# Kernel tuning notes

Hardware: AMD Instinct MI355X
Metric: run time of the kernel (lower is better)

Reference implementation:

```python
import jax, jax.numpy as jnp
import numpy as np

N, D = 65536, 512

def setup_inputs() -> dict:
    key = jax.random.key(0)
    k1, k2, k3, k4, k5 = jax.random.split(key, 5)
    lim = 1.0 / np.sqrt(D)
    inputs = jax.random.normal(k1, (N, D), dtype=jnp.float32)
    key_w = jax.random.uniform(k2, (1, D), minval=-lim, maxval=lim, dtype=jnp.float32)
    key_b = jax.random.uniform(k3, (1,), minval=-lim, maxval=lim, dtype=jnp.float32)
    value_w = jax.random.uniform(k4, (D, D), minval=-lim, maxval=lim, dtype=jnp.float32)
    value_b = jax.random.uniform(k5, (D,), minval=-lim, maxval=lim, dtype=jnp.float32)
    return {"inputs": inputs, "key_w": key_w, "key_b": key_b,
            "value_w": value_w, "value_b": value_b}

def reference(inputs, key_w, key_b, value_w, value_b):
    # key: [N,1], value: [N,D] (torch Linear: x @ W.T + b)
    k = inputs @ key_w.T + key_b            # [N,1]
    v = inputs @ value_w.T + value_b        # [N,D]
    # Reassociate (v @ inputs.T) @ k == v @ (inputs.T @ k): avoids O(N^2) intermediate
    s = inputs.T @ k                        # [D,1]
    x = v @ s                               # [N,1]
    return jax.nn.softmax(x, axis=0)        # softmax over nodes (dim=0)
```

## Files before the change

kernel.cpp:

```cpp
#include <hip/hip_runtime.h>
#include <float.h>

#define NROWS 65536
#define DDIM  512

#define WS_S8   0
#define WS_T    4096
#define WS_M    4608
#define WS_SUM  4609
#define WS_HDR_BYTES ((4610) * 4)

__device__ __forceinline__ unsigned encf(float f) {
    unsigned u = __float_as_uint(f);
    return (u & 0x80000000u) ? ~u : (u | 0x80000000u);
}
__device__ __forceinline__ float decf(unsigned e) {
    unsigned u = (e & 0x80000000u) ? (e ^ 0x80000000u) : ~e;
    return __uint_as_float(u);
}

__global__ __launch_bounds__(256) void kA(const float* __restrict__ in,
                                          const float* __restrict__ key_w,
                                          const float* __restrict__ key_b,
                                          float* __restrict__ s8) {
    const int lane = threadIdx.x & 63;
    const int wv   = threadIdx.x >> 6;
    const int gw   = blockIdx.x * 4 + wv;
    const int nw   = gridDim.x * 4;
    const float4* in4 = (const float4*)in;
    const float4* kw4 = (const float4*)key_w;
    const float4 kw0 = kw4[lane];
    const float4 kw1 = kw4[64 + lane];
    const float  kb  = key_b[0];
    float4 a0 = make_float4(0.f, 0.f, 0.f, 0.f);
    float4 a1 = make_float4(0.f, 0.f, 0.f, 0.f);

    for (int row = gw; row < NROWS; row += nw) {
        const float4* r = in4 + (size_t)row * (DDIM / 4);
        float4 v0 = r[lane];
        float4 v1 = r[64 + lane];
        float p = v0.x*kw0.x + v0.y*kw0.y + v0.z*kw0.z + v0.w*kw0.w
                + v1.x*kw1.x + v1.y*kw1.y + v1.z*kw1.z + v1.w*kw1.w;
        #pragma unroll
        for (int o = 32; o > 0; o >>= 1) p += __shfl_xor(p, o, 64);
        const float k = p + kb;
        a0.x += k*v0.x; a0.y += k*v0.y; a0.z += k*v0.z; a0.w += k*v0.w;
        a1.x += k*v1.x; a1.y += k*v1.y; a1.z += k*v1.z; a1.w += k*v1.w;
    }

    __shared__ float sb[4][512];
    sb[wv][4*lane+0]     = a0.x; sb[wv][4*lane+1]     = a0.y;
    sb[wv][4*lane+2]     = a0.z; sb[wv][4*lane+3]     = a0.w;
    sb[wv][256+4*lane+0] = a1.x; sb[wv][256+4*lane+1] = a1.y;
    sb[wv][256+4*lane+2] = a1.z; sb[wv][256+4*lane+3] = a1.w;
    __syncthreads();

    float* dst = s8 + (size_t)(blockIdx.x & 7) * 512;
    int d = threadIdx.x;
    atomicAdd(&dst[d], sb[0][d] + sb[1][d] + sb[2][d] + sb[3][d]);
    d += 256;
    atomicAdd(&dst[d], sb[0][d] + sb[1][d] + sb[2][d] + sb[3][d]);
}

__global__ __launch_bounds__(512) void kB(const float* __restrict__ vw,
                                          const float* __restrict__ s8,
                                          float* __restrict__ t) {
    const int j = threadIdx.x;
    float acc = 0.f;
    #pragma unroll
    for (int ii = 0; ii < 8; ++ii) {
        const int i = blockIdx.x * 8 + ii;
        float si = 0.f;
        #pragma unroll
        for (int c = 0; c < 8; ++c) si += s8[c * 512 + i];
        acc += vw[(size_t)i * 512 + j] * si;
    }
    atomicAdd(&t[j], acc);
}

__global__ __launch_bounds__(256) void kC(const float* __restrict__ in,
                                          const float* __restrict__ t,
                                          float* __restrict__ x,
                                          unsigned* __restrict__ Menc) {
    const int lane = threadIdx.x & 63;
    const int wv   = threadIdx.x >> 6;
    const int gw   = blockIdx.x * 4 + wv;
    const int nw   = gridDim.x * 4;
    const float4* in4 = (const float4*)in;
    const float4* t4  = (const float4*)t;
    const float4 t0 = t4[lane];
    const float4 t1 = t4[64 + lane];
    float xmax = -FLT_MAX;

    for (int row = gw; row < NROWS; row += nw) {
        const float4* r = in4 + (size_t)row * (DDIM / 4);
        float4 v0 = r[lane];
        float4 v1 = r[64 + lane];
        float p = v0.x*t0.x + v0.y*t0.y + v0.z*t0.z + v0.w*t0.w
                + v1.x*t1.x + v1.y*t1.y + v1.z*t1.z + v1.w*t1.w;
        #pragma unroll
        for (int o = 32; o > 0; o >>= 1) p += __shfl_xor(p, o, 64);
        if (lane == 0) x[row] = p;
        xmax = fmaxf(xmax, p);
    }

    __shared__ float mb[4];
    if (lane == 0) mb[wv] = xmax;
    __syncthreads();
    if (threadIdx.x == 0) {
        float m = fmaxf(fmaxf(mb[0], mb[1]), fmaxf(mb[2], mb[3]));
        atomicMax(Menc, encf(m));
    }
}

__global__ __launch_bounds__(256) void kD(const float* __restrict__ x,
                                          const unsigned* __restrict__ Menc,
                                          float* __restrict__ sum) {
    const float M = decf(*Menc);
    float acc = 0.f;
    for (int i = blockIdx.x * blockDim.x + threadIdx.x; i < NROWS;
         i += gridDim.x * blockDim.x)
        acc += expf(x[i] - M);
    #pragma unroll
    for (int o = 32; o > 0; o >>= 1) acc += __shfl_xor(acc, o, 64);
    __shared__ float sb[4];
    if ((threadIdx.x & 63) == 0) sb[threadIdx.x >> 6] = acc;
    __syncthreads();
    if (threadIdx.x == 0) atomicAdd(sum, sb[0] + sb[1] + sb[2] + sb[3]);
}

__global__ __launch_bounds__(256) void kE(float* __restrict__ x,
                                          const unsigned* __restrict__ Menc,
                                          const float* __restrict__ sum) {
    const float M = decf(*Menc);
    const float inv = 1.0f / *sum;
    for (int i = blockIdx.x * blockDim.x + threadIdx.x; i < NROWS;
         i += gridDim.x * blockDim.x)
        x[i] = expf(x[i] - M) * inv;
}

extern "C" void kernel_launch(void* const* d_in, const int* in_sizes, int n_in,
                              void* d_out, int out_size, void* d_ws, size_t ws_size,
                              hipStream_t stream) {
    const float* in    = (const float*)d_in[0];
    const float* key_w = (const float*)d_in[1];
    const float* key_b = (const float*)d_in[2];
    const float* vw    = (const float*)d_in[3];

    float* ws  = (float*)d_ws;
    float* s8  = ws + WS_S8;
    float* t   = ws + WS_T;
    unsigned* Menc = (unsigned*)(ws + WS_M);
    float* sum = ws + WS_SUM;
    float* x   = (float*)d_out;

    hipMemsetAsync(d_ws, 0, WS_HDR_BYTES, stream);
    kA<<<1024, 256, 0, stream>>>(in, key_w, key_b, s8);
    kB<<<64, 512, 0, stream>>>(vw, s8, t);
    kC<<<1024, 256, 0, stream>>>(in, t, x, Menc);
    kD<<<64, 256, 0, stream>>>(x, Menc, sum);
    kE<<<256, 256, 0, stream>>>(x, Menc, sum);
}
```

Measured before the change: 234.4 us.

## Fuse all stages into one cooperative kernel with grid-wide syncs

Replaces the memset and five separate kernel launches with a single cooperative launch of 1024 blocks that uses grid.sync between phases. Per-block partial sums are written to workspace and reduced deterministically instead of through atomics, and each block handles a contiguous chunk of rows. Launch gaps and the memset are removed, in exchange for several grid-wide barriers, a 1024x512 partial buffer that must be reduced, and a grid that must be fully co-resident. The later phases also switch expf to __expf.

Result: slower. 767.3 us (+227.4%).

```diff
diff --git a/kernel.cpp b/kernel.cpp
--- a/kernel.cpp
+++ b/kernel.cpp
@@ -1,14 +1,14 @@
 #include <hip/hip_runtime.h>
+#include <hip/hip_cooperative_groups.h>
 #include <float.h>
+
+namespace cg = cooperative_groups;
 
 #define NROWS 65536
 #define DDIM  512
+#define NBLK  1024
+#define ROWS_PER_BLK (NROWS / NBLK)
 
-#define WS_S8   0
-#define WS_T    4096
-#define WS_M    4608
-#define WS_SUM  4609
-#define WS_HDR_BYTES ((4610) * 4)
 
 __device__ __forceinline__ unsigned encf(float f) {
     unsigned u = __float_as_uint(f);
@@ -19,124 +19,141 @@
     return __uint_as_float(u);
 }
 
-__global__ __launch_bounds__(256) void kA(const float* __restrict__ in,
-                                          const float* __restrict__ key_w,
-                                          const float* __restrict__ key_b,
-                                          float* __restrict__ s8) {
-    const int lane = threadIdx.x & 63;
-    const int wv   = threadIdx.x >> 6;
-    const int gw   = blockIdx.x * 4 + wv;
-    const int nw   = gridDim.x * 4;
+__global__ __launch_bounds__(256, 4) void fused(const float* __restrict__ in,
+                                                const float* __restrict__ key_w,
+                                                const float* __restrict__ key_b,
+                                                const float* __restrict__ vw,
+                                                float* __restrict__ ws,
+                                                float* __restrict__ out) {
+    cg::grid_group grid = cg::this_grid();
+    const int tid  = threadIdx.x;
+    const int lane = tid & 63;
+    const int wv   = tid >> 6;
+    const int blk  = blockIdx.x;
+
+    float*    spart = ws;
+    float*    s     = ws + (size_t)NBLK * DDIM;
+    float*    t     = s + DDIM;
+    unsigned* Menc  = (unsigned*)(t + DDIM);
+    float*    sum   = (float*)(Menc + 1);
+
+    __shared__ float sb[4][DDIM];
+    __shared__ float red[4];
+
     const float4* in4 = (const float4*)in;
-    const float4* kw4 = (const float4*)key_w;
-    const float4 kw0 = kw4[lane];
-    const float4 kw1 = kw4[64 + lane];
-    const float  kb  = key_b[0];
-    float4 a0 = make_float4(0.f, 0.f, 0.f, 0.f);
-    float4 a1 = make_float4(0.f, 0.f, 0.f, 0.f);
+    const int base = blk * ROWS_PER_BLK;
 
-    for (int row = gw; row < NROWS; row += nw) {
-        const float4* r = in4 + (size_t)row * (DDIM / 4);
-        float4 v0 = r[lane];
-        float4 v1 = r[64 + lane];
-        float p = v0.x*kw0.x + v0.y*kw0.y + v0.z*kw0.z + v0.w*kw0.w
-                + v1.x*kw1.x + v1.y*kw1.y + v1.z*kw1.z + v1.w*kw1.w;
-        #pragma unroll
-        for (int o = 32; o > 0; o >>= 1) p += __shfl_xor(p, o, 64);
-        const float k = p + kb;
-        a0.x += k*v0.x; a0.y += k*v0.y; a0.z += k*v0.z; a0.w += k*v0.w;
-        a1.x += k*v1.x; a1.y += k*v1.y; a1.z += k*v1.z; a1.w += k*v1.w;
+    {
+        const float4* kw4 = (const float4*)key_w;
+        const float4 kw0 = kw4[lane];
+        const float4 kw1 = kw4[64 + lane];
+        const float  kb  = key_b[0];
+        float4 a0 = make_float4(0.f, 0.f, 0.f, 0.f);
+        float4 a1 = make_float4(0.f, 0.f, 0.f, 0.f);
+        for (int i = 0; i < ROWS_PER_BLK / 4; ++i) {
+            const int row = base + 4 * i + wv;
+            const float4* r = in4 + (size_t)row * (DDIM / 4);
+            float4 v0 = r[lane];
+            float4 v1 = r[64 + lane];
+            float p = v0.x*kw0.x + v0.y*kw0.y + v0.z*kw0.z + v0.w*kw0.w
+                    + v1.x*kw1.x + v1.y*kw1.y + v1.z*kw1.z + v1.w*kw1.w;
+            #pragma unroll
+            for (int o = 32; o > 0; o >>= 1) p += __shfl_xor(p, o, 64);
+            const float k = p + kb;
+            a0.x += k*v0.x; a0.y += k*v0.y; a0.z += k*v0.z; a0.w += k*v0.w;
+            a1.x += k*v1.x; a1.y += k*v1.y; a1.z += k*v1.z; a1.w += k*v1.w;
+        }
+        sb[wv][4*lane+0]     = a0.x; sb[wv][4*lane+1]     = a0.y;
+        sb[wv][4*lane+2]     = a0.z; sb[wv][4*lane+3]     = a0.w;
+        sb[wv][256+4*lane+0] = a1.x; sb[wv][256+4*lane+1] = a1.y;
+        sb[wv][256+4*lane+2] = a1.z; sb[wv][256+4*lane+3] = a1.w;
+        __syncthreads();
+        float* dst = spart + (size_t)blk * DDIM;
+        dst[tid]       = sb[0][tid]     + sb[1][tid]     + sb[2][tid]     + sb[3][tid];
+        dst[tid + 256] = sb[0][tid+256] + sb[1][tid+256] + sb[2][tid+256] + sb[3][tid+256];
     }
 
-    __shared__ float sb[4][512];
-    sb[wv][4*lane+0]     = a0.x; sb[wv][4*lane+1]     = a0.y;
-    sb[wv][4*lane+2]     = a0.z; sb[wv][4*lane+3]     = a0.w;
-    sb[wv][256+4*lane+0] = a1.x; sb[wv][256+4*lane+1] = a1.y;
-    sb[wv][256+4*lane+2] = a1.z; sb[wv][256+4*lane+3] = a1.w;
-    __syncthreads();
+    grid.sync();
 
-    float* dst = s8 + (size_t)(blockIdx.x & 7) * 512;
-    int d = threadIdx.x;
-    atomicAdd(&dst[d], sb[0][d] + sb[1][d] + sb[2][d] + sb[3][d]);
-    d += 256;
-    atomicAdd(&dst[d], sb[0][d] + sb[1][d] + sb[2][d] + sb[3][d]);
-}
-
-__global__ __launch_bounds__(512) void kB(const float* __restrict__ vw,
-                                          const float* __restrict__ s8,
-                                          float* __restrict__ t) {
-    const int j = threadIdx.x;
-    float acc = 0.f;
-    #pragma unroll
-    for (int ii = 0; ii < 8; ++ii) {
-        const int i = blockIdx.x * 8 + ii;
-        float si = 0.f;
+    if (blk < DDIM) {
+        const int d = blk;
+        float acc = 0.f;
         #pragma unroll
-        for (int c = 0; c < 8; ++c) si += s8[c * 512 + i];
-        acc += vw[(size_t)i * 512 + j] * si;
-    }
-    atomicAdd(&t[j], acc);
-}
-
-__global__ __launch_bounds__(256) void kC(const float* __restrict__ in,
-                                          const float* __restrict__ t,
-                                          float* __restrict__ x,
-                                          unsigned* __restrict__ Menc) {
-    const int lane = threadIdx.x & 63;
-    const int wv   = threadIdx.x >> 6;
-    const int gw   = blockIdx.x * 4 + wv;
-    const int nw   = gridDim.x * 4;
-    const float4* in4 = (const float4*)in;
-    const float4* t4  = (const float4*)t;
-    const float4 t0 = t4[lane];
-    const float4 t1 = t4[64 + lane];
-    float xmax = -FLT_MAX;
-
-    for (int row = gw; row < NROWS; row += nw) {
-        const float4* r = in4 + (size_t)row * (DDIM / 4);
-        float4 v0 = r[lane];
-        float4 v1 = r[64 + lane];
-        float p = v0.x*t0.x + v0.y*t0.y + v0.z*t0.z + v0.w*t0.w
-                + v1.x*t1.x + v1.y*t1.y + v1.z*t1.z + v1.w*t1.w;
+        for (int m = 0; m < 4; ++m)
+            acc += spart[(size_t)(4 * tid + m) * DDIM + d];
         #pragma unroll
-        for (int o = 32; o > 0; o >>= 1) p += __shfl_xor(p, o, 64);
-        if (lane == 0) x[row] = p;
-        xmax = fmaxf(xmax, p);
+        for (int o = 32; o > 0; o >>= 1) acc += __shfl_xor(acc, o, 64);
+        if (lane == 0) red[wv] = acc;
+        __syncthreads();
+        if (tid == 0) s[d] = red[0] + red[1] + red[2] + red[3];
+    } else if (blk == DDIM && tid == 0) {
+        *Menc = encf(-FLT_MAX);
+        *sum  = 0.f;
     }
 
-    __shared__ float mb[4];
-    if (lane == 0) mb[wv] = xmax;
-    __syncthreads();
-    if (threadIdx.x == 0) {
-        float m = fmaxf(fmaxf(mb[0], mb[1]), fmaxf(mb[2], mb[3]));
-        atomicMax(Menc, encf(m));
+    grid.sync();
+
+    if (blk < DDIM) {
+        const int j = blk;
+        float acc = vw[(size_t)tid * DDIM + j] * s[tid]
+                  + vw[(size_t)(tid + 256) * DDIM + j] * s[tid + 256];
+        #pragma unroll
+        for (int o = 32; o > 0; o >>= 1) acc += __shfl_xor(acc, o, 64);
+        if (lane == 0) red[wv] = acc;
+        __syncthreads();
+        if (tid == 0) t[j] = red[0] + red[1] + red[2] + red[3];
     }
-}
 
-__global__ __launch_bounds__(256) void kD(const float* __restrict__ x,
-                                          const unsigned* __restrict__ Menc,
-                                          float* __restrict__ sum) {
-    const float M = decf(*Menc);
-    float acc = 0.f;
-    for (int i = blockIdx.x * blockDim.x + threadIdx.x; i < NROWS;
-         i += gridDim.x * blockDim.x)
-        acc += expf(x[i] - M);
-    #pragma unroll
-    for (int o = 32; o > 0; o >>= 1) acc += __shfl_xor(acc, o, 64);
-    __shared__ float sb[4];
-    if ((threadIdx.x & 63) == 0) sb[threadIdx.x >> 6] = acc;
-    __syncthreads();
-    if (threadIdx.x == 0) atomicAdd(sum, sb[0] + sb[1] + sb[2] + sb[3]);
-}
+    grid.sync();
 
-__global__ __launch_bounds__(256) void kE(float* __restrict__ x,
-                                          const unsigned* __restrict__ Menc,
-                                          const float* __restrict__ sum) {
-    const float M = decf(*Menc);
-    const float inv = 1.0f / *sum;
-    for (int i = blockIdx.x * blockDim.x + threadIdx.x; i < NROWS;
-         i += gridDim.x * blockDim.x)
-        x[i] = expf(x[i] - M) * inv;
+    {
+        const float4* t4 = (const float4*)t;
+        const float4 t0 = t4[lane];
+        const float4 t1 = t4[64 + lane];
+        float xmax = -FLT_MAX;
+        for (int i = 0; i < ROWS_PER_BLK / 4; ++i) {
+            const int row = base + 4 * i + wv;
+            const float4* r = in4 + (size_t)row * (DDIM / 4);
+            float4 v0 = r[lane];
+            float4 v1 = r[64 + lane];
+            float p = v0.x*t0.x + v0.y*t0.y + v0.z*t0.z + v0.w*t0.w
+                    + v1.x*t1.x + v1.y*t1.y + v1.z*t1.z + v1.w*t1.w;
+            #pragma unroll
+            for (int o = 32; o > 0; o >>= 1) p += __shfl_xor(p, o, 64);
+            if (lane == 0) out[row] = p;
+            xmax = fmaxf(xmax, p);
+        }
+        __syncthreads();
+        if (lane == 0) red[wv] = xmax;
+        __syncthreads();
+        if (tid == 0) {
+            float m = fmaxf(fmaxf(red[0], red[1]), fmaxf(red[2], red[3]));
+            atomicMax(Menc, encf(m));
+        }
+    }
+
+    grid.sync();
+
+    if (blk < 256) {
+        const float M = decf(*Menc);
+        const int i = blk * 256 + tid;
+        float e = __expf(out[i] - M);
+        float acc = e;
+        #pragma unroll
+        for (int o = 32; o > 0; o >>= 1) acc += __shfl_xor(acc, o, 64);
+        if (lane == 0) red[wv] = acc;
+        __syncthreads();
+        if (tid == 0) atomicAdd(sum, red[0] + red[1] + red[2] + red[3]);
+    }
+
+    grid.sync();
+
+    if (blk < 256) {
+        const float M   = decf(*Menc);
+        const float inv = 1.0f / *sum;
+        const int i = blk * 256 + tid;
+        out[i] = __expf(out[i] - M) * inv;
+    }
 }
 
 extern "C" void kernel_launch(void* const* d_in, const int* in_sizes, int n_in,
@@ -148,16 +165,9 @@
     const float* vw    = (const float*)d_in[3];
 
     float* ws  = (float*)d_ws;
-    float* s8  = ws + WS_S8;
-    float* t   = ws + WS_T;
-    unsigned* Menc = (unsigned*)(ws + WS_M);
-    float* sum = ws + WS_SUM;
-    float* x   = (float*)d_out;
+    float* out = (float*)d_out;
 
-    hipMemsetAsync(d_ws, 0, WS_HDR_BYTES, stream);
-    kA<<<1024, 256, 0, stream>>>(in, key_w, key_b, s8);
-    kB<<<64, 512, 0, stream>>>(vw, s8, t);
-    kC<<<1024, 256, 0, stream>>>(in, t, x, Menc);
-    kD<<<64, 256, 0, stream>>>(x, Menc, sum);
-    kE<<<256, 256, 0, stream>>>(x, Menc, sum);
+    void* args[] = {(void*)&in, (void*)&key_w, (void*)&key_b, (void*)&vw,
+                    (void*)&ws, (void*)&out};
+    hipLaunchCooperativeKernel((void*)fused, dim3(NBLK), dim3(256), args, 0, stream);
 }
```

## Fuse softmax max/sum into matvec pass and restructure row loads per wave

Applied to the files above, without the earlier changes.

Each wave now handles 16 contiguous rows, with four rows in flight per wave (16 lanes per row, 8 float4 loads per lane) instead of one row per iteration, to raise memory-level parallelism. The kC pass computes an online softmax (running max and rescaled sum) per block and writes per-block partials. This removes the separate sum-of-exponentials kernel and the atomic max. The final kernel merges the 1024 partials per block and normalises, at the cost of redundant partial merging in every block and more register pressure. Occupancy hints are added through launch bounds.

Result: faster. 221.0 us (-5.7%).

```diff
diff --git a/kernel.cpp b/kernel.cpp
--- a/kernel.cpp
+++ b/kernel.cpp
@@ -4,62 +4,82 @@
 #define NROWS 65536
 #define DDIM  512
 
-#define WS_S8   0
-#define WS_T    4096
-#define WS_M    4608
-#define WS_SUM  4609
-#define WS_HDR_BYTES ((4610) * 4)
-
-__device__ __forceinline__ unsigned encf(float f) {
-    unsigned u = __float_as_uint(f);
-    return (u & 0x80000000u) ? ~u : (u | 0x80000000u);
-}
-__device__ __forceinline__ float decf(unsigned e) {
-    unsigned u = (e & 0x80000000u) ? (e ^ 0x80000000u) : ~e;
-    return __uint_as_float(u);
-}
-
-__global__ __launch_bounds__(256) void kA(const float* __restrict__ in,
-                                          const float* __restrict__ key_w,
-                                          const float* __restrict__ key_b,
-                                          float* __restrict__ s8) {
-    const int lane = threadIdx.x & 63;
-    const int wv   = threadIdx.x >> 6;
+#define WS_T       4096
+#define WS_MP      4608
+#define WS_LP      5632
+#define WS_ZERO_BYTES (4608 * 4)
+
+__global__ __launch_bounds__(256, 3) void kA(const float* __restrict__ in,
+                                             const float* __restrict__ key_w,
+                                             const float* __restrict__ key_b,
+                                             float* __restrict__ s8) {
+    const int tid  = threadIdx.x;
+    const int lane = tid & 63;
+    const int wv   = tid >> 6;
+    const int q    = lane >> 4;
+    const int u    = lane & 15;
     const int gw   = blockIdx.x * 4 + wv;
-    const int nw   = gridDim.x * 4;
-    const float4* in4 = (const float4*)in;
+
     const float4* kw4 = (const float4*)key_w;
-    const float4 kw0 = kw4[lane];
-    const float4 kw1 = kw4[64 + lane];
-    const float  kb  = key_b[0];
-    float4 a0 = make_float4(0.f, 0.f, 0.f, 0.f);
-    float4 a1 = make_float4(0.f, 0.f, 0.f, 0.f);
-
-    for (int row = gw; row < NROWS; row += nw) {
-        const float4* r = in4 + (size_t)row * (DDIM / 4);
-        float4 v0 = r[lane];
-        float4 v1 = r[64 + lane];
-        float p = v0.x*kw0.x + v0.y*kw0.y + v0.z*kw0.z + v0.w*kw0.w
-                + v1.x*kw1.x + v1.y*kw1.y + v1.z*kw1.z + v1.w*kw1.w;
-        #pragma unroll
-        for (int o = 32; o > 0; o >>= 1) p += __shfl_xor(p, o, 64);
+    float4 kw[8];
+    #pragma unroll
+    for (int j = 0; j < 8; ++j) kw[j] = kw4[u + j * 16];
+    const float kb = key_b[0];
+
+    float4 acc[8];
+    #pragma unroll
+    for (int j = 0; j < 8; ++j) acc[j] = make_float4(0.f, 0.f, 0.f, 0.f);
+
+    const int rowbase = gw * 16;
+    #pragma unroll
+    for (int it = 0; it < 4; ++it) {
+        const int row = rowbase + it * 4 + q;
+        const float4* r4 = (const float4*)(in + (size_t)row * DDIM);
+        float4 v[8];
+        #pragma unroll
+        for (int j = 0; j < 8; ++j) v[j] = r4[u + j * 16];
+        float p = 0.f;
+        #pragma unroll
+        for (int j = 0; j < 8; ++j)
+            p += v[j].x * kw[j].x + v[j].y * kw[j].y
+               + v[j].z * kw[j].z + v[j].w * kw[j].w;
+        #pragma unroll
+        for (int o = 1; o < 16; o <<= 1) p += __shfl_xor(p, o, 64);
         const float k = p + kb;
-        a0.x += k*v0.x; a0.y += k*v0.y; a0.z += k*v0.z; a0.w += k*v0.w;
-        a1.x += k*v1.x; a1.y += k*v1.y; a1.z += k*v1.z; a1.w += k*v1.w;
-    }
-
-    __shared__ float sb[4][512];
-    sb[wv][4*lane+0]     = a0.x; sb[wv][4*lane+1]     = a0.y;
-    sb[wv][4*lane+2]     = a0.z; sb[wv][4*lane+3]     = a0.w;
-    sb[wv][256+4*lane+0] = a1.x; sb[wv][256+4*lane+1] = a1.y;
-    sb[wv][256+4*lane+2] = a1.z; sb[wv][256+4*lane+3] = a1.w;
-    __syncthreads();
-
-    float* dst = s8 + (size_t)(blockIdx.x & 7) * 512;
-    int d = threadIdx.x;
-    atomicAdd(&dst[d], sb[0][d] + sb[1][d] + sb[2][d] + sb[3][d]);
-    d += 256;
-    atomicAdd(&dst[d], sb[0][d] + sb[1][d] + sb[2][d] + sb[3][d]);
+        #pragma unroll
+        for (int j = 0; j < 8; ++j) {
+            acc[j].x += k * v[j].x; acc[j].y += k * v[j].y;
+            acc[j].z += k * v[j].z; acc[j].w += k * v[j].w;
+        }
+    }
+
+    #pragma unroll
+    for (int o = 16; o < 64; o <<= 1) {
+        #pragma unroll
+        for (int j = 0; j < 8; ++j) {
+            acc[j].x += __shfl_xor(acc[j].x, o, 64);
+            acc[j].y += __shfl_xor(acc[j].y, o, 64);
+            acc[j].z += __shfl_xor(acc[j].z, o, 64);
+            acc[j].w += __shfl_xor(acc[j].w, o, 64);
+        }
+    }
+
+    __shared__ float sb[4][DDIM];
+    if (q == 0) {
+        #pragma unroll
+        for (int j = 0; j < 8; ++j) {
+            const int c = u * 4 + j * 64;
+            sb[wv][c]     = acc[j].x;
+            sb[wv][c + 1] = acc[j].y;
+            sb[wv][c + 2] = acc[j].z;
+            sb[wv][c + 3] = acc[j].w;
+        }
+    }
+    __syncthreads();
+
+    float* dst = s8 + (size_t)(blockIdx.x & 7) * DDIM;
+    atomicAdd(&dst[tid],       sb[0][tid]     + sb[1][tid]     + sb[2][tid]     + sb[3][tid]);
+    atomicAdd(&dst[tid + 256], sb[0][tid+256] + sb[1][tid+256] + sb[2][tid+256] + sb[3][tid+256]);
 }
 
 __global__ __launch_bounds__(512) void kB(const float* __restrict__ vw,
@@ -78,65 +98,110 @@
     atomicAdd(&t[j], acc);
 }
 
-__global__ __launch_bounds__(256) void kC(const float* __restrict__ in,
-                                          const float* __restrict__ t,
-                                          float* __restrict__ x,
-                                          unsigned* __restrict__ Menc) {
-    const int lane = threadIdx.x & 63;
-    const int wv   = threadIdx.x >> 6;
+__global__ __launch_bounds__(256, 4) void kC(const float* __restrict__ in,
+                                             const float* __restrict__ t,
+                                             float* __restrict__ x,
+                                             float* __restrict__ mpart,
+                                             float* __restrict__ lpart) {
+    const int tid  = threadIdx.x;
+    const int lane = tid & 63;
+    const int wv   = tid >> 6;
+    const int q    = lane >> 4;
+    const int u    = lane & 15;
     const int gw   = blockIdx.x * 4 + wv;
-    const int nw   = gridDim.x * 4;
-    const float4* in4 = (const float4*)in;
-    const float4* t4  = (const float4*)t;
-    const float4 t0 = t4[lane];
-    const float4 t1 = t4[64 + lane];
-    float xmax = -FLT_MAX;
-
-    for (int row = gw; row < NROWS; row += nw) {
-        const float4* r = in4 + (size_t)row * (DDIM / 4);
-        float4 v0 = r[lane];
-        float4 v1 = r[64 + lane];
-        float p = v0.x*t0.x + v0.y*t0.y + v0.z*t0.z + v0.w*t0.w
-                + v1.x*t1.x + v1.y*t1.y + v1.z*t1.z + v1.w*t1.w;
-        #pragma unroll
-        for (int o = 32; o > 0; o >>= 1) p += __shfl_xor(p, o, 64);
-        if (lane == 0) x[row] = p;
-        xmax = fmaxf(xmax, p);
-    }
-
-    __shared__ float mb[4];
-    if (lane == 0) mb[wv] = xmax;
-    __syncthreads();
-    if (threadIdx.x == 0) {
-        float m = fmaxf(fmaxf(mb[0], mb[1]), fmaxf(mb[2], mb[3]));
-        atomicMax(Menc, encf(m));
-    }
-}
-
-__global__ __launch_bounds__(256) void kD(const float* __restrict__ x,
-                                          const unsigned* __restrict__ Menc,
-                                          float* __restrict__ sum) {
-    const float M = decf(*Menc);
-    float acc = 0.f;
-    for (int i = blockIdx.x * blockDim.x + threadIdx.x; i < NROWS;
-         i += gridDim.x * blockDim.x)
-        acc += expf(x[i] - M);
-    #pragma unroll
-    for (int o = 32; o > 0; o >>= 1) acc += __shfl_xor(acc, o, 64);
-    __shared__ float sb[4];
-    if ((threadIdx.x & 63) == 0) sb[threadIdx.x >> 6] = acc;
-    __syncthreads();
-    if (threadIdx.x == 0) atomicAdd(sum, sb[0] + sb[1] + sb[2] + sb[3]);
+
+    const float4* t4 = (const float4*)t;
+    float4 tt[8];
+    #pragma unroll
+    for (int j = 0; j < 8; ++j) tt[j] = t4[u + j * 16];
+
+    float m = -FLT_MAX, l = 0.f;
+    const int rowbase = gw * 16;
+    #pragma unroll
+    for (int it = 0; it < 4; ++it) {
+        const int row = rowbase + it * 4 + q;
+        const float4* r4 = (const float4*)(in + (size_t)row * DDIM);
+        float4 v[8];
+        #pragma unroll
+        for (int j = 0; j < 8; ++j) v[j] = r4[u + j * 16];
+        float p = 0.f;
+        #pragma unroll
+        for (int j = 0; j < 8; ++j)
+            p += v[j].x * tt[j].x + v[j].y * tt[j].y
+               + v[j].z * tt[j].z + v[j].w * tt[j].w;
+        #pragma unroll
+        for (int o = 1; o < 16; o <<= 1) p += __shfl_xor(p, o, 64);
+        if (u == 0) x[row] = p;
+        const float mn = fmaxf(m, p);
+        l = l * __expf(m - mn) + __expf(p - mn);
+        m = mn;
+    }
+
+    #pragma unroll
+    for (int o = 16; o < 64; o <<= 1) {
+        const float mo = __shfl_xor(m, o, 64);
+        const float lo = __shfl_xor(l, o, 64);
+        const float mn = fmaxf(m, mo);
+        l = l * __expf(m - mn) + lo * __expf(mo - mn);
+        m = mn;
+    }
+    __shared__ float ms[4], ls[4];
+    if (lane == 0) { ms[wv] = m; ls[wv] = l; }
+    __syncthreads();
+    if (tid == 0) {
+        m = ms[0]; l = ls[0];
+        #pragma unroll
+        for (int w = 1; w < 4; ++w) {
+            const float mn = fmaxf(m, ms[w]);
+            l = l * __expf(m - mn) + ls[w] * __expf(ms[w] - mn);
+            m = mn;
+        }
+        mpart[blockIdx.x] = m;
+        lpart[blockIdx.x] = l;
+    }
 }
 
 __global__ __launch_bounds__(256) void kE(float* __restrict__ x,
-                                          const unsigned* __restrict__ Menc,
-                                          const float* __restrict__ sum) {
-    const float M = decf(*Menc);
-    const float inv = 1.0f / *sum;
-    for (int i = blockIdx.x * blockDim.x + threadIdx.x; i < NROWS;
-         i += gridDim.x * blockDim.x)
-        x[i] = expf(x[i] - M) * inv;
+                                          const float* __restrict__ mpart,
+                                          const float* __restrict__ lpart) {
+    const int tid  = threadIdx.x;
+    const int lane = tid & 63;
+    const int wv   = tid >> 6;
+
+    float m = -FLT_MAX, l = 0.f;
+    #pragma unroll
+    for (int j = 0; j < 4; ++j) {
+        const float mp = mpart[tid * 4 + j];
+        const float lp = lpart[tid * 4 + j];
+        const float mn = fmaxf(m, mp);
+        l = l * __expf(m - mn) + lp * __expf(mp - mn);
+        m = mn;
+    }
+    #pragma unroll
+    for (int o = 1; o < 64; o <<= 1) {
+        const float mo = __shfl_xor(m, o, 64);
+        const float lo = __shfl_xor(l, o, 64);
+        const float mn = fmaxf(m, mo);
+        l = l * __expf(m - mn) + lo * __expf(mo - mn);
+        m = mn;
+    }
+    __shared__ float ms[4], ls[4];
+    __shared__ float Ms, Ls;
+    if (lane == 0) { ms[wv] = m; ls[wv] = l; }
+    __syncthreads();
+    if (tid == 0) {
+        m = ms[0]; l = ls[0];
+        #pragma unroll
+        for (int w = 1; w < 4; ++w) {
+            const float mn = fmaxf(m, ms[w]);
+            l = l * __expf(m - mn) + ls[w] * __expf(ms[w] - mn);
+            m = mn;
+        }
+        Ms = m; Ls = l;
+    }
+    __syncthreads();
+    const int i = blockIdx.x * 256 + tid;
+    x[i] = __expf(x[i] - Ms) / Ls;
 }
 
 extern "C" void kernel_launch(void* const* d_in, const int* in_sizes, int n_in,
@@ -147,17 +212,16 @@
     const float* key_b = (const float*)d_in[2];
     const float* vw    = (const float*)d_in[3];
 
-    float* ws  = (float*)d_ws;
-    float* s8  = ws + WS_S8;
-    float* t   = ws + WS_T;
-    unsigned* Menc = (unsigned*)(ws + WS_M);
-    float* sum = ws + WS_SUM;
-    float* x   = (float*)d_out;
-
-    hipMemsetAsync(d_ws, 0, WS_HDR_BYTES, stream);
+    float* ws    = (float*)d_ws;
+    float* s8    = ws;
+    float* t     = ws + WS_T;
+    float* mpart = ws + WS_MP;
+    float* lpart = ws + WS_LP;
+    float* out   = (float*)d_out;
+
+    hipMemsetAsync(d_ws, 0, WS_ZERO_BYTES, stream);
     kA<<<1024, 256, 0, stream>>>(in, key_w, key_b, s8);
     kB<<<64, 512, 0, stream>>>(vw, s8, t);
-    kC<<<1024, 256, 0, stream>>>(in, t, x, Menc);
-    kD<<<64, 256, 0, stream>>>(x, Menc, sum);
-    kE<<<256, 256, 0, stream>>>(x, Menc, sum);
-}
+    kC<<<1024, 256, 0, stream>>>(in, t, out, mpart, lpart);
+    kE<<<256, 256, 0, stream>>>(out, mpart, lpart);
+}
```
